# Optimization experiments

Measured on AMD Instinct MI355X. Metric: run time of the kernel, lower is better.

## Reference

```python
import jax, jax.numpy as jnp
import numpy as np

N_NODES = 100000
N_EDGES = 1600000
HID = 64
BN_EPS = 1e-5


def _glorot(key, shape):
    fan_in, fan_out = shape[0], shape[1]
    lim = np.sqrt(6.0 / (fan_in + fan_out))
    return jax.random.uniform(key, shape, jnp.float32, -lim, lim)


def setup_inputs() -> dict:
    key = jax.random.key(0)
    ks = jax.random.split(key, 16)
    inp = {
        "x": jax.random.normal(ks[0], (N_NODES, HID), jnp.float32),
        "edge_index": jax.random.randint(ks[1], (2, N_EDGES), 0, N_NODES, jnp.int64),
        "edge_attr": jax.random.normal(ks[2], (N_EDGES,), jnp.float32),
    }
    # per-layer GIN MLP params: Linear(in,hid) -> BN(hid) -> ReLU -> Linear(hid,out)
    for i in range(2):
        inp[f"W1_{i}"] = _glorot(ks[3 + 5 * i], (HID, HID))
        inp[f"b1_{i}"] = jnp.zeros((HID,), jnp.float32)
        inp[f"gamma_{i}"] = jnp.ones((HID,), jnp.float32)
        inp[f"beta_{i}"] = jnp.zeros((HID,), jnp.float32)
        inp[f"W2_{i}"] = _glorot(ks[4 + 5 * i], (HID, HID))
        inp[f"b2_{i}"] = jnp.zeros((HID,), jnp.float32)
    inp["Wjk"] = _glorot(ks[14], (3 * HID, HID))
    inp["bjk"] = jnp.zeros((HID,), jnp.float32)
    return inp


def _gin_conv(x, src, dst, W1, b1, gamma, beta, W2, b2):
    # GIN aggregation: (1 + eps) * x + sum_{j->i} x_j, eps = 0
    agg = jax.ops.segment_sum(x[src], dst, num_segments=N_NODES)  # [N, d]
    h = (x + agg) @ W1 + b1
    # BatchNorm1d over node dimension (training-style batch statistics)
    mean = jnp.mean(h, axis=0)
    var = jnp.var(h, axis=0)
    h = gamma * (h - mean) * jax.lax.rsqrt(var + BN_EPS) + beta
    h = jax.nn.relu(h)
    return h @ W2 + b2


def reference(x, edge_index, edge_attr,
              W1_0, b1_0, gamma_0, beta_0, W2_0, b2_0,
              W1_1, b1_1, gamma_1, beta_1, W2_1, b2_1,
              Wjk, bjk):
    # edge_attr is accepted but ignored (torch_geometric GINConv does not use it)
    src, dst = edge_index[0], edge_index[1]
    xs = [x]
    h = x
    params = [(W1_0, b1_0, gamma_0, beta_0, W2_0, b2_0),
              (W1_1, b1_1, gamma_1, beta_1, W2_1, b2_1)]
    for p in params:
        h = _gin_conv(h, src, dst, *p)
        h = jax.nn.relu(h)  # dropout p=0.0 is identity
        xs.append(h)
    return jnp.concatenate(xs, axis=-1) @ Wjk + bjk
```

## Files before the change

kernel.cpp:

```cpp
#include <hip/hip_runtime.h>

#define N_NODES 100000
#define N_EDGES 1600000
#define HID 64
#define BN_EPS 1e-5f

#define GATHER_BLOCKS (N_NODES / 32)

#define ROW_TILES (N_NODES / 16)
#define TPW1 4
#define G1_BLOCKS ((ROW_TILES + 4*TPW1 - 1) / (4*TPW1))
#define TPW2 2
#define G2_BLOCKS ((ROW_TILES + 4*TPW2 - 1) / (4*TPW2))

#define NB 391
#define MS_BLOCKS 1000
#define MS_EPB (N_EDGES / MS_BLOCKS)
#define MS_CNT (NB * MS_BLOCKS)
#define GS_CHUNK 512
#define GS_BLOCKS ((MS_CNT + GS_CHUNK - 1) / GS_CHUNK)

#define CVT_B 3125
#define WT_B 112
#define PREP_BLOCKS (CVT_B + WT_B + MS_BLOCKS)

typedef __bf16 bf16x8 __attribute__((ext_vector_type(8)));
typedef float  f32x4  __attribute__((ext_vector_type(4)));
typedef unsigned short u16x8 __attribute__((ext_vector_type(8)));

__device__ __forceinline__ float bf2f(unsigned short u) {
    return __uint_as_float(((unsigned)u) << 16);
}
__device__ __forceinline__ unsigned short f2bf_rne(float f) {
    unsigned u = __float_as_uint(f);
    u += 0x7FFFu + ((u >> 16) & 1u);
    return (unsigned short)(u >> 16);
}

__global__ __launch_bounds__(256) void prep_kernel(
        const float* __restrict__ x, unsigned short* __restrict__ xb,
        const float* __restrict__ Wjk,
        const float* __restrict__ W1_0, const float* __restrict__ W2_0,
        const float* __restrict__ W1_1, const float* __restrict__ W2_1,
        unsigned short* __restrict__ wjk_t,
        unsigned short* __restrict__ w1t_0, unsigned short* __restrict__ w2t_0,
        unsigned short* __restrict__ w1t_1, unsigned short* __restrict__ w2t_1,
        const int* __restrict__ dst, int* __restrict__ cnt) {
    __shared__ int h[NB];
    const int b = blockIdx.x;
    if (b < CVT_B) {
        size_t i = ((size_t)b * 256 + threadIdx.x) * 8;
        float4 a = *reinterpret_cast<const float4*>(x + i);
        float4 c = *reinterpret_cast<const float4*>(x + i + 4);
        ushort4 w0 = make_ushort4(f2bf_rne(a.x), f2bf_rne(a.y), f2bf_rne(a.z), f2bf_rne(a.w));
        ushort4 w1 = make_ushort4(f2bf_rne(c.x), f2bf_rne(c.y), f2bf_rne(c.z), f2bf_rne(c.w));
        *reinterpret_cast<ushort4*>(xb + i) = w0;
        *reinterpret_cast<ushort4*>(xb + i + 4) = w1;
    } else if (b < CVT_B + WT_B) {
        int i = (b - CVT_B) * 256 + threadIdx.x;
        if (i < 12288) {
            int c = i / 192, k = i - c * 192;
            wjk_t[i] = f2bf_rne(Wjk[k * 64 + c]);
        } else {
            int r = i - 12288;
            int which = r >> 12, rem = r & 4095;
            int c = rem >> 6, k = rem & 63;
            const float* W = (which == 0) ? W1_0 : (which == 1) ? W2_0
                           : (which == 2) ? W1_1 : W2_1;
            unsigned short* Wt = (which == 0) ? w1t_0 : (which == 1) ? w2t_0
                               : (which == 2) ? w1t_1 : w2t_1;
            Wt[rem] = f2bf_rne(W[k * 64 + c]);
        }
    } else {
        const int hb = b - CVT_B - WT_B;
        for (int i = threadIdx.x; i < NB; i += 256) h[i] = 0;
        __syncthreads();
        const int e0 = hb * MS_EPB;
        for (int e = e0 + threadIdx.x; e < e0 + MS_EPB; e += 256)
            atomicAdd(&h[dst[e] >> 8], 1);
        __syncthreads();
        for (int i = threadIdx.x; i < NB; i += 256)
            cnt[i * MS_BLOCKS + hb] = h[i];
    }
}

__global__ __launch_bounds__(256) void scan_partial_g(
        const int* __restrict__ in, int* __restrict__ out,
        int* __restrict__ bsums, int n) {
    __shared__ int sd[256];
    int t = threadIdx.x;
    int base = blockIdx.x * GS_CHUNK;
    int i0 = base + 2 * t, i1 = i0 + 1;
    int d0 = (i0 < n) ? in[i0] : 0;
    int d1 = (i1 < n) ? in[i1] : 0;
    sd[t] = d0 + d1;
    __syncthreads();
    for (int o = 1; o < 256; o <<= 1) {
        int v = (t >= o) ? sd[t - o] : 0;
        __syncthreads();
        sd[t] += v;
        __syncthreads();
    }
    int excl = sd[t] - (d0 + d1);
    if (i0 < n) out[i0] = excl;
    if (i1 < n) out[i1] = excl + d0;
    if (t == 255) bsums[blockIdx.x] = sd[255];
}

__global__ __launch_bounds__(256) void scan_bsums_kernel(int* __restrict__ bsums, int nb) {
    __shared__ int sd[256];
    int t = threadIdx.x;
    int v[4]; int s = 0;
#pragma unroll
    for (int k = 0; k < 4; ++k) {
        int i = t * 4 + k;
        v[k] = (i < nb) ? bsums[i] : 0;
        s += v[k];
    }
    sd[t] = s;
    __syncthreads();
    for (int o = 1; o < 256; o <<= 1) {
        int u = (t >= o) ? sd[t - o] : 0;
        __syncthreads();
        sd[t] += u;
        __syncthreads();
    }
    int run = sd[t] - s;
#pragma unroll
    for (int k = 0; k < 4; ++k) {
        int i = t * 4 + k;
        if (i < nb) bsums[i] = run;
        run += v[k];
    }
}

__global__ __launch_bounds__(256) void scan_addback_g(
        int* __restrict__ out, const int* __restrict__ bsums, int n, int total) {
    int t = threadIdx.x;
    int b = bsums[blockIdx.x];
    int base = blockIdx.x * GS_CHUNK;
    int i0 = base + 2 * t, i1 = i0 + 1;
    if (i0 < n) out[i0] += b;
    if (i1 < n) out[i1] += b;
    if (blockIdx.x == 0 && t == 0) out[n] = total;
}

__global__ __launch_bounds__(256) void msplit_scatter_kernel(
        const int* __restrict__ src, const int* __restrict__ dst,
        const int* __restrict__ psum, int* __restrict__ bucketed) {
    __shared__ int cur[NB];
    for (int i = threadIdx.x; i < NB; i += 256)
        cur[i] = psum[i * MS_BLOCKS + blockIdx.x];
    __syncthreads();
    const int e0 = blockIdx.x * MS_EPB;
    for (int e = e0 + threadIdx.x; e < e0 + MS_EPB; e += 256) {
        int d = dst[e];
        int p = atomicAdd(&cur[d >> 8], 1);
        bucketed[p] = (src[e] << 8) | (d & 255);
    }
}

__global__ __launch_bounds__(256) void bucket_csr_kernel(
        const int* __restrict__ bucketed, const int* __restrict__ psum,
        int* __restrict__ off, int* __restrict__ eidx) {
    const int j = blockIdx.x;
    const int t = threadIdx.x;
    __shared__ int deg[256];
    __shared__ int sd[256];
    __shared__ int base_s, size_s;
    if (t == 0) {
        int b = psum[j * MS_BLOCKS];
        int nxt = (j == NB - 1) ? N_EDGES : psum[(j + 1) * MS_BLOCKS];
        base_s = b; size_s = nxt - b;
    }
    deg[t] = 0;
    __syncthreads();
    const int base = base_s, size = size_s;
    const int nlo = j << 8;
    for (int i = t; i < size; i += 256)
        atomicAdd(&deg[(unsigned)bucketed[base + i] & 255u], 1);
    __syncthreads();
    int d0 = deg[t];
    sd[t] = d0;
    __syncthreads();
    for (int o = 1; o < 256; o <<= 1) {
        int v = (t >= o) ? sd[t - o] : 0;
        __syncthreads();
        sd[t] += v;
        __syncthreads();
    }
    int excl = sd[t] - d0;
    int g0 = nlo + t;
    if (g0 <= N_NODES) off[g0] = base + excl;
    __syncthreads();
    deg[t] = excl;
    __syncthreads();
    for (int i = t; i < size; i += 256) {
        unsigned e = (unsigned)bucketed[base + i];
        int p = atomicAdd(&deg[e & 255u], 1);
        eidx[base + p] = (int)(e >> 8);
    }
}

__global__ __launch_bounds__(256) void gather_kernel(
        const unsigned short* __restrict__ xb, const int* __restrict__ off,
        const int* __restrict__ eidx, unsigned short* __restrict__ aggb) {
    const int lane = threadIdx.x & 63;
    const int g    = lane >> 3;
    const int col  = (lane & 7) << 3;
    const int w    = threadIdx.x >> 6;
    const int n = blockIdx.x * 32 + w * 8 + g;

    const int beg = off[n], end = off[n + 1];
    bf16x8 s8 = *reinterpret_cast<const bf16x8*>(xb + (size_t)n * HID + col);
    float acc[8];
#pragma unroll
    for (int i = 0; i < 8; ++i) acc[i] = (float)s8[i];

    int j = beg;
    for (; j + 4 <= end; j += 4) {
        int s0 = eidx[j], s1 = eidx[j + 1], s2 = eidx[j + 2], s3 = eidx[j + 3];
        bf16x8 r0 = *reinterpret_cast<const bf16x8*>(xb + (size_t)s0 * HID + col);
        bf16x8 r1 = *reinterpret_cast<const bf16x8*>(xb + (size_t)s1 * HID + col);
        bf16x8 r2 = *reinterpret_cast<const bf16x8*>(xb + (size_t)s2 * HID + col);
        bf16x8 r3 = *reinterpret_cast<const bf16x8*>(xb + (size_t)s3 * HID + col);
#pragma unroll
        for (int i = 0; i < 8; ++i)
            acc[i] += ((float)r0[i] + (float)r1[i]) + ((float)r2[i] + (float)r3[i]);
    }
    for (; j < end; ++j) {
        int s0 = eidx[j];
        bf16x8 r0 = *reinterpret_cast<const bf16x8*>(xb + (size_t)s0 * HID + col);
#pragma unroll
        for (int i = 0; i < 8; ++i) acc[i] += (float)r0[i];
    }

    u16x8 o;
#pragma unroll
    for (int i = 0; i < 8; ++i) o[i] = f2bf_rne(acc[i]);
    *reinterpret_cast<u16x8*>(aggb + (size_t)n * HID + col) = o;
}

__global__ __launch_bounds__(256) void gemm1_mfma_kernel(
        const unsigned short* __restrict__ aggb, const unsigned short* __restrict__ W1t,
        const float* __restrict__ bias, unsigned short* __restrict__ hb,
        float* __restrict__ stats_partial) {
    const int lane = threadIdx.x & 63;
    const int l15 = lane & 15, lhi = lane >> 4;
    const int w = threadIdx.x >> 6;

    bf16x8 bfrag[2][4];
    float bs[4];
#pragma unroll
    for (int f = 0; f < 4; ++f) {
        const unsigned short* wp = W1t + (size_t)(f * 16 + l15) * 64 + lhi * 8;
        bfrag[0][f] = *reinterpret_cast<const bf16x8*>(wp);
        bfrag[1][f] = *reinterpret_cast<const bf16x8*>(wp + 32);
        bs[f] = bias[f * 16 + l15];
    }

    float ssum[4] = {0.f, 0.f, 0.f, 0.f}, ssq[4] = {0.f, 0.f, 0.f, 0.f};

    const int tile0 = (blockIdx.x * 4 + w) * TPW1;
#pragma unroll
    for (int tt = 0; tt < TPW1; ++tt) {
        const int tile = tile0 + tt;
        if (tile < ROW_TILES) {
            const int r0 = tile * 16;
            const size_t arow = (size_t)(r0 + l15) * 64 + lhi * 8;
            bf16x8 a0 = *reinterpret_cast<const bf16x8*>(aggb + arow);
            bf16x8 a1 = *reinterpret_cast<const bf16x8*>(aggb + arow + 32);
            f32x4 acc[4];
#pragma unroll
            for (int f = 0; f < 4; ++f) acc[f] = (f32x4){bs[f], bs[f], bs[f], bs[f]};
#pragma unroll
            for (int f = 0; f < 4; ++f) {
                acc[f] = __builtin_amdgcn_mfma_f32_16x16x32_bf16(a0, bfrag[0][f], acc[f], 0, 0, 0);
                acc[f] = __builtin_amdgcn_mfma_f32_16x16x32_bf16(a1, bfrag[1][f], acc[f], 0, 0, 0);
            }
#pragma unroll
            for (int f = 0; f < 4; ++f)
#pragma unroll
                for (int i = 0; i < 4; ++i) {
                    hb[(size_t)(r0 + lhi * 4 + i) * 64 + f * 16 + l15] = f2bf_rne(acc[f][i]);
                    ssum[f] += acc[f][i];
                    ssq[f]  += acc[f][i] * acc[f][i];
                }
        }
    }

    __shared__ float red[2][4][256];
#pragma unroll
    for (int f = 0; f < 4; ++f) {
        red[0][f][threadIdx.x] = ssum[f];
        red[1][f][threadIdx.x] = ssq[f];
    }
    __syncthreads();
    if (threadIdx.x < 64) {
        int c = threadIdx.x, f = c >> 4, p = c & 15;
        float s = 0.f, q = 0.f;
#pragma unroll
        for (int u = 0; u < 16; ++u) {
            int t = (u >> 2) * 64 + (u & 3) * 16 + p;
            s += red[0][f][t];
            q += red[1][f][t];
        }
        stats_partial[(size_t)blockIdx.x * 128 + c]      = s;
        stats_partial[(size_t)blockIdx.x * 128 + 64 + c] = q;
    }
}

__global__ __launch_bounds__(256) void bn_gemm_mfma_kernel(
        const unsigned short* __restrict__ hb, const unsigned short* __restrict__ W2t,
        const float* __restrict__ bias, const float* __restrict__ scale,
        const float* __restrict__ shift, unsigned short* __restrict__ outb) {
    const int lane = threadIdx.x & 63;
    const int l15 = lane & 15, lhi = lane >> 4;
    const int w = threadIdx.x >> 6;

    bf16x8 bfrag[2][4];
    float bs[4];
#pragma unroll
    for (int f = 0; f < 4; ++f) {
        const unsigned short* wp = W2t + (size_t)(f * 16 + l15) * 64 + lhi * 8;
        bfrag[0][f] = *reinterpret_cast<const bf16x8*>(wp);
        bfrag[1][f] = *reinterpret_cast<const bf16x8*>(wp + 32);
        bs[f] = bias[f * 16 + l15];
    }
    float sc[2][8], sh[2][8];
#pragma unroll
    for (int t = 0; t < 2; ++t)
#pragma unroll
        for (int j = 0; j < 8; ++j) {
            int k = t * 32 + lhi * 8 + j;
            sc[t][j] = scale[k];
            sh[t][j] = shift[k];
        }

    const int tile0 = (blockIdx.x * 4 + w) * TPW2;
#pragma unroll
    for (int tt = 0; tt < TPW2; ++tt) {
        const int tile = tile0 + tt;
        if (tile >= ROW_TILES) return;
        const int r0 = tile * 16;
        f32x4 acc[4];
#pragma unroll
        for (int f = 0; f < 4; ++f) acc[f] = (f32x4){bs[f], bs[f], bs[f], bs[f]};
#pragma unroll
        for (int t = 0; t < 2; ++t) {
            const unsigned short* hp = hb + (size_t)(r0 + l15) * 64 + t * 32 + lhi * 8;
            bf16x8 raw = *reinterpret_cast<const bf16x8*>(hp);
            bf16x8 a;
#pragma unroll
            for (int j = 0; j < 8; ++j)
                a[j] = (__bf16)fmaxf(fmaf(sc[t][j], (float)raw[j], sh[t][j]), 0.f);
#pragma unroll
            for (int f = 0; f < 4; ++f)
                acc[f] = __builtin_amdgcn_mfma_f32_16x16x32_bf16(a, bfrag[t][f], acc[f], 0, 0, 0);
        }
#pragma unroll
        for (int f = 0; f < 4; ++f)
#pragma unroll
            for (int i = 0; i < 4; ++i)
                outb[(size_t)(r0 + lhi * 4 + i) * 64 + f * 16 + l15] =
                    f2bf_rne(fmaxf(acc[f][i], 0.f));
    }
}

#define LT_STRIDE 88
__global__ __launch_bounds__(256) void bn_gemm_jumphead_kernel(
        const unsigned short* __restrict__ hb, const unsigned short* __restrict__ W2t,
        const float* __restrict__ bias2, const float* __restrict__ scale,
        const float* __restrict__ shift,
        const unsigned short* __restrict__ xb, const unsigned short* __restrict__ h1b,
        const unsigned short* __restrict__ Wt, const float* __restrict__ bjk,
        float* __restrict__ out) {
    __shared__ unsigned short lt[4][16 * LT_STRIDE];
    const int lane = threadIdx.x & 63;
    const int l15 = lane & 15, lhi = lane >> 4;
    const int w = threadIdx.x >> 6;

    bf16x8 b2frag[2][4];
    float bs2[4];
#pragma unroll
    for (int f = 0; f < 4; ++f) {
        const unsigned short* wp = W2t + (size_t)(f * 16 + l15) * 64 + lhi * 8;
        b2frag[0][f] = *reinterpret_cast<const bf16x8*>(wp);
        b2frag[1][f] = *reinterpret_cast<const bf16x8*>(wp + 32);
        bs2[f] = bias2[f * 16 + l15];
    }
    float sc[2][8], sh[2][8];
#pragma unroll
    for (int t = 0; t < 2; ++t)
#pragma unroll
        for (int j = 0; j < 8; ++j) {
            int k = t * 32 + lhi * 8 + j;
            sc[t][j] = scale[k];
            sh[t][j] = shift[k];
        }
    bf16x8 bjfrag[6][4];
    float bsj[4];
#pragma unroll
    for (int f = 0; f < 4; ++f) {
        const unsigned short* wp = Wt + (size_t)(f * 16 + l15) * 192 + lhi * 8;
#pragma unroll
        for (int t = 0; t < 6; ++t)
            bjfrag[t][f] = *reinterpret_cast<const bf16x8*>(wp + t * 32);
        bsj[f] = bjk[f * 16 + l15];
    }

    const int tile0 = (blockIdx.x * 4 + w) * TPW2;
#pragma unroll
    for (int tt = 0; tt < TPW2; ++tt) {
        const int tile = tile0 + tt;
        if (tile >= ROW_TILES) return;
        const int r0 = tile * 16;

        f32x4 acc2[4];
#pragma unroll
        for (int f = 0; f < 4; ++f) acc2[f] = (f32x4){bs2[f], bs2[f], bs2[f], bs2[f]};
#pragma unroll
        for (int t = 0; t < 2; ++t) {
            const unsigned short* hp = hb + (size_t)(r0 + l15) * 64 + t * 32 + lhi * 8;
            bf16x8 raw = *reinterpret_cast<const bf16x8*>(hp);
            bf16x8 a;
#pragma unroll
            for (int j = 0; j < 8; ++j)
                a[j] = (__bf16)fmaxf(fmaf(sc[t][j], (float)raw[j], sh[t][j]), 0.f);
#pragma unroll
            for (int f = 0; f < 4; ++f)
                acc2[f] = __builtin_amdgcn_mfma_f32_16x16x32_bf16(a, b2frag[t][f], acc2[f], 0, 0, 0);
        }
#pragma unroll
        for (int f = 0; f < 4; ++f)
#pragma unroll
            for (int i = 0; i < 4; ++i)
                lt[w][(lhi * 4 + i) * LT_STRIDE + f * 16 + l15] =
                    f2bf_rne(fmaxf(acc2[f][i], 0.f));
        bf16x8 a4 = *reinterpret_cast<const bf16x8*>(&lt[w][l15 * LT_STRIDE + lhi * 8]);
        bf16x8 a5 = *reinterpret_cast<const bf16x8*>(&lt[w][l15 * LT_STRIDE + 32 + lhi * 8]);

        const size_t arow = (size_t)(r0 + l15) * 64 + lhi * 8;
        bf16x8 a0 = *reinterpret_cast<const bf16x8*>(xb + arow);
        bf16x8 a1 = *reinterpret_cast<const bf16x8*>(xb + arow + 32);
        bf16x8 a2 = *reinterpret_cast<const bf16x8*>(h1b + arow);
        bf16x8 a3 = *reinterpret_cast<const bf16x8*>(h1b + arow + 32);
        f32x4 accj[4];
#pragma unroll
        for (int f = 0; f < 4; ++f) accj[f] = (f32x4){bsj[f], bsj[f], bsj[f], bsj[f]};
#pragma unroll
        for (int f = 0; f < 4; ++f) {
            accj[f] = __builtin_amdgcn_mfma_f32_16x16x32_bf16(a0, bjfrag[0][f], accj[f], 0, 0, 0);
            accj[f] = __builtin_amdgcn_mfma_f32_16x16x32_bf16(a1, bjfrag[1][f], accj[f], 0, 0, 0);
            accj[f] = __builtin_amdgcn_mfma_f32_16x16x32_bf16(a2, bjfrag[2][f], accj[f], 0, 0, 0);
            accj[f] = __builtin_amdgcn_mfma_f32_16x16x32_bf16(a3, bjfrag[3][f], accj[f], 0, 0, 0);
            accj[f] = __builtin_amdgcn_mfma_f32_16x16x32_bf16(a4, bjfrag[4][f], accj[f], 0, 0, 0);
            accj[f] = __builtin_amdgcn_mfma_f32_16x16x32_bf16(a5, bjfrag[5][f], accj[f], 0, 0, 0);
        }
#pragma unroll
        for (int f = 0; f < 4; ++f)
#pragma unroll
            for (int i = 0; i < 4; ++i)
                out[(size_t)(r0 + lhi * 4 + i) * 64 + f * 16 + l15] = accj[f][i];
    }
}

__global__ __launch_bounds__(1024) void bn_finalize_kernel(
        const float* __restrict__ stats_partial, int nblocks,
        const float* __restrict__ gamma, const float* __restrict__ beta,
        float* __restrict__ scale, float* __restrict__ shift) {
    __shared__ float red[2][1024];
    const int t = threadIdx.x;
    const int c = t & 63;
    const int chunk = t >> 6;
    float s = 0.f, q = 0.f;
    for (int b = chunk; b < nblocks; b += 16) {
        s += stats_partial[(size_t)b * 128 + c];
        q += stats_partial[(size_t)b * 128 + 64 + c];
    }
    red[0][t] = s;
    red[1][t] = q;
    __syncthreads();
    if (chunk == 0) {
        float ss = 0.f, qq = 0.f;
#pragma unroll
        for (int k = 0; k < 16; ++k) {
            ss += red[0][k * 64 + c];
            qq += red[1][k * 64 + c];
        }
        float mean = ss / (float)N_NODES;
        float var  = qq / (float)N_NODES - mean * mean;
        float scl  = gamma[c] * rsqrtf(var + BN_EPS);
        scale[c] = scl;
        shift[c] = beta[c] - mean * scl;
    }
}

extern "C" void kernel_launch(void* const* d_in, const int* in_sizes, int n_in,
                              void* d_out, int out_size, void* d_ws, size_t ws_size,
                              hipStream_t stream) {
    const float* x    = (const float*)d_in[0];
    const int*   ei   = (const int*)d_in[1];
    const int*   src  = ei;
    const int*   dst  = ei + N_EDGES;
    const float* W1_0 = (const float*)d_in[3];
    const float* b1_0 = (const float*)d_in[4];
    const float* g_0  = (const float*)d_in[5];
    const float* be_0 = (const float*)d_in[6];
    const float* W2_0 = (const float*)d_in[7];
    const float* b2_0 = (const float*)d_in[8];
    const float* W1_1 = (const float*)d_in[9];
    const float* b1_1 = (const float*)d_in[10];
    const float* g_1  = (const float*)d_in[11];
    const float* be_1 = (const float*)d_in[12];
    const float* W2_1 = (const float*)d_in[13];
    const float* b2_1 = (const float*)d_in[14];
    const float* Wjk  = (const float*)d_in[15];
    const float* bjk  = (const float*)d_in[16];

    const size_t FEAT = (size_t)N_NODES * HID;

    unsigned short* aggb = (unsigned short*)d_ws;
    unsigned short* hb   = aggb + FEAT;
    unsigned short* xb   = hb + FEAT;
    unsigned short* h1b  = xb + FEAT;
    int*   bucketed = (int*)(h1b + FEAT);
    float* stats = (float*)(bucketed + N_EDGES);
    float* scale = stats + (size_t)G1_BLOCKS * 128;
    float* shift = scale + 64;
    int*   off   = (int*)(shift + 64);
    int*   eidx  = off + N_NODES + 2;
    int*   cnt   = eidx + N_EDGES;
    int*   psum  = cnt + MS_CNT;
    int*   bsums = psum + MS_CNT + 2;
    unsigned short* wjk_t = (unsigned short*)(bsums + 1024);
    unsigned short* w2t_0 = wjk_t + 64 * 192;
    unsigned short* w2t_1 = w2t_0 + 64 * 64;
    unsigned short* w1t_0 = w2t_1 + 64 * 64;
    unsigned short* w1t_1 = w1t_0 + 64 * 64;
    float* out   = (float*)d_out;

    prep_kernel<<<PREP_BLOCKS, 256, 0, stream>>>(
        x, xb, Wjk, W1_0, W2_0, W1_1, W2_1,
        wjk_t, w1t_0, w2t_0, w1t_1, w2t_1, dst, cnt);

    scan_partial_g<<<GS_BLOCKS, 256, 0, stream>>>(cnt, psum, bsums, MS_CNT);
    scan_bsums_kernel<<<1, 256, 0, stream>>>(bsums, GS_BLOCKS);
    scan_addback_g<<<GS_BLOCKS, 256, 0, stream>>>(psum, bsums, MS_CNT, N_EDGES);
    msplit_scatter_kernel<<<MS_BLOCKS, 256, 0, stream>>>(src, dst, psum, bucketed);
    bucket_csr_kernel<<<NB, 256, 0, stream>>>(bucketed, psum, off, eidx);

    gather_kernel<<<GATHER_BLOCKS, 256, 0, stream>>>(xb, off, eidx, aggb);
    gemm1_mfma_kernel<<<G1_BLOCKS, 256, 0, stream>>>(aggb, w1t_0, b1_0, hb, stats);
    bn_finalize_kernel<<<1, 1024, 0, stream>>>(stats, G1_BLOCKS, g_0, be_0, scale, shift);
    bn_gemm_mfma_kernel<<<G2_BLOCKS, 256, 0, stream>>>(hb, w2t_0, b2_0, scale, shift, h1b);

    gather_kernel<<<GATHER_BLOCKS, 256, 0, stream>>>(h1b, off, eidx, aggb);
    gemm1_mfma_kernel<<<G1_BLOCKS, 256, 0, stream>>>(aggb, w1t_1, b1_1, hb, stats);
    bn_finalize_kernel<<<1, 1024, 0, stream>>>(stats, G1_BLOCKS, g_1, be_1, scale, shift);
    bn_gemm_jumphead_kernel<<<G2_BLOCKS, 256, 0, stream>>>(
        hb, w2t_1, b2_1, scale, shift, xb, h1b, wjk_t, bjk, out);
}
```

Baseline: 190.3 us.

## Fuse neighbor gather with first GIN linear layer through shared memory

```diff
diff --git a/kernel.cpp b/kernel.cpp
--- a/kernel.cpp
+++ b/kernel.cpp
@@ -5,11 +5,9 @@
 #define HID 64
 #define BN_EPS 1e-5f
 
-#define GATHER_BLOCKS (N_NODES / 32)
+#define GG_BLOCKS (N_NODES / 32)
 
 #define ROW_TILES (N_NODES / 16)
-#define TPW1 4
-#define G1_BLOCKS ((ROW_TILES + 4*TPW1 - 1) / (4*TPW1))
 #define TPW2 2
 #define G2_BLOCKS ((ROW_TILES + 4*TPW2 - 1) / (4*TPW2))
 
@@ -23,6 +21,8 @@
 #define CVT_B 3125
 #define WT_B 112
 #define PREP_BLOCKS (CVT_B + WT_B + MS_BLOCKS)
+
+#define LDS_STRIDE 72
 
 typedef __bf16 bf16x8 __attribute__((ext_vector_type(8)));
 typedef float  f32x4  __attribute__((ext_vector_type(4)));
@@ -202,105 +202,110 @@
     }
 }
 
-__global__ __launch_bounds__(256) void gather_kernel(
+__global__ __launch_bounds__(256) void gather_gemm1_kernel(
         const unsigned short* __restrict__ xb, const int* __restrict__ off,
-        const int* __restrict__ eidx, unsigned short* __restrict__ aggb) {
+        const int* __restrict__ eidx, const unsigned short* __restrict__ W1t,
+        const float* __restrict__ bias, unsigned short* __restrict__ hb,
+        float* __restrict__ stats_partial) {
+    __shared__ unsigned short agg[32 * LDS_STRIDE];
+    __shared__ float red[2][4][128];
     const int lane = threadIdx.x & 63;
     const int g    = lane >> 3;
     const int col  = (lane & 7) << 3;
     const int w    = threadIdx.x >> 6;
-    const int n = blockIdx.x * 32 + w * 8 + g;
-
-    const int beg = off[n], end = off[n + 1];
-    bf16x8 s8 = *reinterpret_cast<const bf16x8*>(xb + (size_t)n * HID + col);
-    float acc[8];
-#pragma unroll
-    for (int i = 0; i < 8; ++i) acc[i] = (float)s8[i];
-
-    int j = beg;
-    for (; j + 4 <= end; j += 4) {
-        int s0 = eidx[j], s1 = eidx[j + 1], s2 = eidx[j + 2], s3 = eidx[j + 3];
-        bf16x8 r0 = *reinterpret_cast<const bf16x8*>(xb + (size_t)s0 * HID + col);
-        bf16x8 r1 = *reinterpret_cast<const bf16x8*>(xb + (size_t)s1 * HID + col);
-        bf16x8 r2 = *reinterpret_cast<const bf16x8*>(xb + (size_t)s2 * HID + col);
-        bf16x8 r3 = *reinterpret_cast<const bf16x8*>(xb + (size_t)s3 * HID + col);
-#pragma unroll
-        for (int i = 0; i < 8; ++i)
-            acc[i] += ((float)r0[i] + (float)r1[i]) + ((float)r2[i] + (float)r3[i]);
-    }
-    for (; j < end; ++j) {
-        int s0 = eidx[j];
-        bf16x8 r0 = *reinterpret_cast<const bf16x8*>(xb + (size_t)s0 * HID + col);
-#pragma unroll
-        for (int i = 0; i < 8; ++i) acc[i] += (float)r0[i];
-    }
-
-    u16x8 o;
-#pragma unroll
-    for (int i = 0; i < 8; ++i) o[i] = f2bf_rne(acc[i]);
-    *reinterpret_cast<u16x8*>(aggb + (size_t)n * HID + col) = o;
-}
-
-__global__ __launch_bounds__(256) void gemm1_mfma_kernel(
-        const unsigned short* __restrict__ aggb, const unsigned short* __restrict__ W1t,
-        const float* __restrict__ bias, unsigned short* __restrict__ hb,
-        float* __restrict__ stats_partial) {
-    const int lane = threadIdx.x & 63;
+    const int row  = w * 8 + g;
+    const int n    = blockIdx.x * 32 + row;
+
+    {
+        const int beg = off[n], end = off[n + 1];
+        bf16x8 s8 = *reinterpret_cast<const bf16x8*>(xb + (size_t)n * HID + col);
+        float acc[8];
+#pragma unroll
+        for (int i = 0; i < 8; ++i) acc[i] = (float)s8[i];
+        int j = beg;
+        for (; j + 8 <= end; j += 8) {
+            int s0 = eidx[j],     s1 = eidx[j + 1], s2 = eidx[j + 2], s3 = eidx[j + 3];
+            int s4 = eidx[j + 4], s5 = eidx[j + 5], s6 = eidx[j + 6], s7 = eidx[j + 7];
+            bf16x8 r0 = *reinterpret_cast<const bf16x8*>(xb + (size_t)s0 * HID + col);
+            bf16x8 r1 = *reinterpret_cast<const bf16x8*>(xb + (size_t)s1 * HID + col);
+            bf16x8 r2 = *reinterpret_cast<const bf16x8*>(xb + (size_t)s2 * HID + col);
+            bf16x8 r3 = *reinterpret_cast<const bf16x8*>(xb + (size_t)s3 * HID + col);
+            bf16x8 r4 = *reinterpret_cast<const bf16x8*>(xb + (size_t)s4 * HID + col);
+            bf16x8 r5 = *reinterpret_cast<const bf16x8*>(xb + (size_t)s5 * HID + col);
+            bf16x8 r6 = *reinterpret_cast<const bf16x8*>(xb + (size_t)s6 * HID + col);
+            bf16x8 r7 = *reinterpret_cast<const bf16x8*>(xb + (size_t)s7 * HID + col);
+#pragma unroll
+            for (int i = 0; i < 8; ++i)
+                acc[i] += (((float)r0[i] + (float)r1[i]) + ((float)r2[i] + (float)r3[i]))
+                        + (((float)r4[i] + (float)r5[i]) + ((float)r6[i] + (float)r7[i]));
+        }
+        if (j + 4 <= end) {
+            int s0 = eidx[j], s1 = eidx[j + 1], s2 = eidx[j + 2], s3 = eidx[j + 3];
+            bf16x8 r0 = *reinterpret_cast<const bf16x8*>(xb + (size_t)s0 * HID + col);
+            bf16x8 r1 = *reinterpret_cast<const bf16x8*>(xb + (size_t)s1 * HID + col);
+            bf16x8 r2 = *reinterpret_cast<const bf16x8*>(xb + (size_t)s2 * HID + col);
+            bf16x8 r3 = *reinterpret_cast<const bf16x8*>(xb + (size_t)s3 * HID + col);
+#pragma unroll
+            for (int i = 0; i < 8; ++i)
+                acc[i] += ((float)r0[i] + (float)r1[i]) + ((float)r2[i] + (float)r3[i]);
+            j += 4;
+        }
+        for (; j < end; ++j) {
+            int s0 = eidx[j];
+            bf16x8 r0 = *reinterpret_cast<const bf16x8*>(xb + (size_t)s0 * HID + col);
+#pragma unroll
+            for (int i = 0; i < 8; ++i) acc[i] += (float)r0[i];
+        }
+        u16x8 o;
+#pragma unroll
+        for (int i = 0; i < 8; ++i) o[i] = f2bf_rne(acc[i]);
+        *reinterpret_cast<u16x8*>(&agg[row * LDS_STRIDE + col]) = o;
+    }
+    __syncthreads();
+
     const int l15 = lane & 15, lhi = lane >> 4;
-    const int w = threadIdx.x >> 6;
-
-    bf16x8 bfrag[2][4];
-    float bs[4];
-#pragma unroll
-    for (int f = 0; f < 4; ++f) {
-        const unsigned short* wp = W1t + (size_t)(f * 16 + l15) * 64 + lhi * 8;
-        bfrag[0][f] = *reinterpret_cast<const bf16x8*>(wp);
-        bfrag[1][f] = *reinterpret_cast<const bf16x8*>(wp + 32);
-        bs[f] = bias[f * 16 + l15];
-    }
-
-    float ssum[4] = {0.f, 0.f, 0.f, 0.f}, ssq[4] = {0.f, 0.f, 0.f, 0.f};
-
-    const int tile0 = (blockIdx.x * 4 + w) * TPW1;
-#pragma unroll
-    for (int tt = 0; tt < TPW1; ++tt) {
-        const int tile = tile0 + tt;
-        if (tile < ROW_TILES) {
-            const int r0 = tile * 16;
-            const size_t arow = (size_t)(r0 + l15) * 64 + lhi * 8;
-            bf16x8 a0 = *reinterpret_cast<const bf16x8*>(aggb + arow);
-            bf16x8 a1 = *reinterpret_cast<const bf16x8*>(aggb + arow + 32);
-            f32x4 acc[4];
-#pragma unroll
-            for (int f = 0; f < 4; ++f) acc[f] = (f32x4){bs[f], bs[f], bs[f], bs[f]};
-#pragma unroll
-            for (int f = 0; f < 4; ++f) {
-                acc[f] = __builtin_amdgcn_mfma_f32_16x16x32_bf16(a0, bfrag[0][f], acc[f], 0, 0, 0);
-                acc[f] = __builtin_amdgcn_mfma_f32_16x16x32_bf16(a1, bfrag[1][f], acc[f], 0, 0, 0);
+    if (w < 2) {
+        bf16x8 bfrag[2][4];
+        float bs[4];
+#pragma unroll
+        for (int f = 0; f < 4; ++f) {
+            const unsigned short* wp = W1t + (size_t)(f * 16 + l15) * 64 + lhi * 8;
+            bfrag[0][f] = *reinterpret_cast<const bf16x8*>(wp);
+            bfrag[1][f] = *reinterpret_cast<const bf16x8*>(wp + 32);
+            bs[f] = bias[f * 16 + l15];
+        }
+        const int r0 = blockIdx.x * 32 + w * 16;
+        const unsigned short* ap = &agg[(w * 16 + l15) * LDS_STRIDE + lhi * 8];
+        bf16x8 a0 = *reinterpret_cast<const bf16x8*>(ap);
+        bf16x8 a1 = *reinterpret_cast<const bf16x8*>(ap + 32);
+        f32x4 acc[4];
+#pragma unroll
+        for (int f = 0; f < 4; ++f) acc[f] = (f32x4){bs[f], bs[f], bs[f], bs[f]};
+#pragma unroll
+        for (int f = 0; f < 4; ++f) {
+            acc[f] = __builtin_amdgcn_mfma_f32_16x16x32_bf16(a0, bfrag[0][f], acc[f], 0, 0, 0);
+            acc[f] = __builtin_amdgcn_mfma_f32_16x16x32_bf16(a1, bfrag[1][f], acc[f], 0, 0, 0);
+        }
+        float ssum[4], ssq[4];
+#pragma unroll
+        for (int f = 0; f < 4; ++f) {
+            ssum[f] = 0.f; ssq[f] = 0.f;
+#pragma unroll
+            for (int i = 0; i < 4; ++i) {
+                hb[(size_t)(r0 + lhi * 4 + i) * 64 + f * 16 + l15] = f2bf_rne(acc[f][i]);
+                ssum[f] += acc[f][i];
+                ssq[f]  += acc[f][i] * acc[f][i];
             }
-#pragma unroll
-            for (int f = 0; f < 4; ++f)
-#pragma unroll
-                for (int i = 0; i < 4; ++i) {
-                    hb[(size_t)(r0 + lhi * 4 + i) * 64 + f * 16 + l15] = f2bf_rne(acc[f][i]);
-                    ssum[f] += acc[f][i];
-                    ssq[f]  += acc[f][i] * acc[f][i];
-                }
-        }
-    }
-
-    __shared__ float red[2][4][256];
-#pragma unroll
-    for (int f = 0; f < 4; ++f) {
-        red[0][f][threadIdx.x] = ssum[f];
-        red[1][f][threadIdx.x] = ssq[f];
+            red[0][f][threadIdx.x] = ssum[f];
+            red[1][f][threadIdx.x] = ssq[f];
+        }
     }
     __syncthreads();
     if (threadIdx.x < 64) {
         int c = threadIdx.x, f = c >> 4, p = c & 15;
         float s = 0.f, q = 0.f;
 #pragma unroll
-        for (int u = 0; u < 16; ++u) {
+        for (int u = 0; u < 8; ++u) {
             int t = (u >> 2) * 64 + (u & 3) * 16 + p;
             s += red[0][f][t];
             q += red[1][f][t];
@@ -520,13 +525,12 @@
 
     const size_t FEAT = (size_t)N_NODES * HID;
 
-    unsigned short* aggb = (unsigned short*)d_ws;
-    unsigned short* hb   = aggb + FEAT;
+    unsigned short* hb   = (unsigned short*)d_ws;
     unsigned short* xb   = hb + FEAT;
     unsigned short* h1b  = xb + FEAT;
     int*   bucketed = (int*)(h1b + FEAT);
     float* stats = (float*)(bucketed + N_EDGES);
-    float* scale = stats + (size_t)G1_BLOCKS * 128;
+    float* scale = stats + (size_t)GG_BLOCKS * 128;
     float* shift = scale + 64;
     int*   off   = (int*)(shift + 64);
     int*   eidx  = off + N_NODES + 2;
@@ -550,14 +554,14 @@
     msplit_scatter_kernel<<<MS_BLOCKS, 256, 0, stream>>>(src, dst, psum, bucketed);
     bucket_csr_kernel<<<NB, 256, 0, stream>>>(bucketed, psum, off, eidx);
 
-    gather_kernel<<<GATHER_BLOCKS, 256, 0, stream>>>(xb, off, eidx, aggb);
-    gemm1_mfma_kernel<<<G1_BLOCKS, 256, 0, stream>>>(aggb, w1t_0, b1_0, hb, stats);
-    bn_finalize_kernel<<<1, 1024, 0, stream>>>(stats, G1_BLOCKS, g_0, be_0, scale, shift);
+    gather_gemm1_kernel<<<GG_BLOCKS, 256, 0, stream>>>(
+        xb, off, eidx, w1t_0, b1_0, hb, stats);
+    bn_finalize_kernel<<<1, 1024, 0, stream>>>(stats, GG_BLOCKS, g_0, be_0, scale, shift);
     bn_gemm_mfma_kernel<<<G2_BLOCKS, 256, 0, stream>>>(hb, w2t_0, b2_0, scale, shift, h1b);
 
-    gather_kernel<<<GATHER_BLOCKS, 256, 0, stream>>>(h1b, off, eidx, aggb);
-    gemm1_mfma_kernel<<<G1_BLOCKS, 256, 0, stream>>>(aggb, w1t_1, b1_1, hb, stats);
-    bn_finalize_kernel<<<1, 1024, 0, stream>>>(stats, G1_BLOCKS, g_1, be_1, scale, shift);
+    gather_gemm1_kernel<<<GG_BLOCKS, 256, 0, stream>>>(
+        h1b, off, eidx, w1t_1, b1_1, hb, stats);
+    bn_finalize_kernel<<<1, 1024, 0, stream>>>(stats, GG_BLOCKS, g_1, be_1, scale, shift);
     bn_gemm_jumphead_kernel<<<G2_BLOCKS, 256, 0, stream>>>(
         hb, w2t_1, b2_1, scale, shift, xb, h1b, wjk_t, bjk, out);
 }
```

After: 278.7 us. 1.46x slower.
